# Performance work log

Measured on AMD Instinct MI355X. Metric: run time of the kernel, lower is better.

## Reference

```python
import jax, jax.numpy as jnp
import numpy as np

LOOKBACK = 512
T = 131072
FEES = 0.00025


def setup_inputs() -> dict:
    key = jax.random.key(0)
    k1, k2, k3, k4 = jax.random.split(key, 4)
    features = jax.random.normal(k1, (T,), dtype=jnp.float32)
    # gross per-step asset returns near 1.0 (hourly price relatives)
    asset_returns = 1.0 + 0.01 * jax.random.normal(k2, (T,), dtype=jnp.float32)
    theta = jax.random.uniform(k3, (LOOKBACK + 2,), dtype=jnp.float32)  # torch.rand init
    p_init = jax.random.uniform(k4, (LOOKBACK - 1,), dtype=jnp.float32)  # the lookback-1 seed positions
    return {"features": features, "asset_returns": asset_returns, "theta": theta, "p_init": p_init}


def _positions(features, theta, p_init):
    lb = theta.shape[0] - 2
    n_steps = features.shape[0] - lb + 1
    # all sliding windows features[t-lb:t], t = lb..T  -> [n_steps, lb]
    idx = jnp.arange(n_steps)[:, None] + jnp.arange(lb)[None, :]
    win = features[idx]
    wmean = win.mean(axis=1, keepdims=True)
    wstd = jnp.std(win, axis=1, ddof=1, keepdims=True)  # torch.std is unbiased
    win_norm = (win - wmean) / wstd

    # running stats over ALL positions so far (growing list in the original)
    n0 = jnp.asarray(p_init.shape[0], dtype=jnp.float32)
    state0 = (n0, p_init.sum(), jnp.sum(p_init * p_init), p_init[-1])

    one = jnp.ones((1,), dtype=features.dtype)

    def step(state, w):
        n, s, ss, p_last = state
        mean = s / n
        std = jnp.sqrt((ss - n * mean * mean) / (n - 1.0))
        last_norm = (p_last - mean) / std
        xt = jnp.concatenate([w, last_norm[None], one])  # [lb+2]
        xt = (xt - xt.mean()) / jnp.std(xt, ddof=1)
        p_new = jax.nn.sigmoid(jnp.dot(theta, xt))
        return (n + 1.0, s + p_new, ss + p_new * p_new, p_new), p_new

    _, p_seq = jax.lax.scan(step, state0, win_norm)
    return jnp.concatenate([p_init, p_seq])  # length T


def _bot_returns(P, asset_returns, fees):
    inv0 = P[0]
    cash0 = 1.0 - inv0

    def step(state, rp):
        inv, cash = state
        r, p = rp
        inv = inv * r
        pv = inv + cash
        delta = pv * p - inv  # desired - current investment
        inv = inv + jnp.where(delta > 0, delta * (1.0 - fees), delta)
        cash = cash + jnp.where(delta > 0, -delta, -delta * (1.0 - fees))
        return (inv, cash), inv + cash

    _, pv_tail = jax.lax.scan(step, (inv0, cash0), (asset_returns[1:], P[1:]))
    pv = jnp.concatenate([jnp.ones((1,), dtype=pv_tail.dtype), pv_tail])  # length T
    ratios = pv[1:] / pv[:-1]
    return jnp.concatenate([jnp.ones((1,), dtype=ratios.dtype), ratios])


def reference(features, asset_returns, theta, p_init):
    P = _positions(features, theta, p_init)
    return _bot_returns(P, asset_returns, FEES)
```

## Files before the change

kernel.cpp:

```cpp
#include <hip/hip_runtime.h>
#include <math.h>

#define T_TOTAL 131072
#define LB      512
#define NSTEPS  130561
#define NPAD    130564
#define OMF     0.99975f
#define KC     -1.4426950408889634f

#define OFF_E    0
#define OFF_P0   (NPAD)
#define OFF_P    (2*NPAD)
#define OFF_BS   (2*NPAD + T_TOTAL)
#define OFF_BSS  (OFF_BS + 2048)
#define OFF_CP   (OFF_BSS + 2048)

static __device__ __forceinline__ float fast_rcp(float x) {
#if __has_builtin(__builtin_amdgcn_rcpf)
    return __builtin_amdgcn_rcpf(x);
#else
    return 1.0f / x;
#endif
}
static __device__ __forceinline__ float fast_rsq(float x) {
#if __has_builtin(__builtin_amdgcn_rsqf)
    return __builtin_amdgcn_rsqf(x);
#else
    return 1.0f / sqrtf(x);
#endif
}
static __device__ __forceinline__ float fast_exp2(float x) {
#if __has_builtin(__builtin_amdgcn_exp2f)
    return __builtin_amdgcn_exp2f(x);
#else
    return exp2f(x);
#endif
}

__global__ __launch_bounds__(256, 1) void precompute_kernel(
    const float* __restrict__ features,
    const float* __restrict__ theta,
    const float* __restrict__ p_init,
    float* __restrict__ e_out,
    float* __restrict__ p0_out,
    float* __restrict__ P,
    float* __restrict__ bs,
    float* __restrict__ bss,
    float* __restrict__ cpool)
{
    __shared__ float f_lds[1536];
    __shared__ float th_lds[512];
    const int tid = threadIdx.x;
    const int b   = blockIdx.x;
    const int base = b * 1024;

    {
        const float4* fg = (const float4*)features;
        float4* f4s = (float4*)f_lds;
        int g0 = b * 256 + tid; g0 = g0 > 32767 ? 32767 : g0;
        f4s[tid] = fg[g0];
        if (tid < 128) {
            int g1 = b * 256 + 256 + tid; g1 = g1 > 32767 ? 32767 : g1;
            f4s[256 + tid] = fg[g1];
        }
        const float4* tg = (const float4*)theta;
        float4* t4s = (float4*)th_lds;
        if (tid >= 128 && tid < 256) t4s[tid - 128] = tg[tid - 128];
    }
    if (b == 0) {
        P[tid] = p_init[tid < 511 ? tid : 510];
        if (tid + 256 < 511) P[tid + 256] = p_init[tid + 256];
    }
    __syncthreads();

    float thsum = 0.f;
    {
        int l6 = tid & 63;
#pragma unroll
        for (int j = 0; j < 8; ++j) thsum += th_lds[l6 + 64 * j];
#pragma unroll
        for (int d = 32; d; d >>= 1) thsum += __shfl_xor(thsum, d, 64);
    }

    const float4* f4 = (const float4*)f_lds;
    const float4* t4 = (const float4*)th_lds;

    float d0 = 0.f, d1 = 0.f, d2 = 0.f, d3 = 0.f;
    float fsum0 = 0.f, fss0 = 0.f;
    float4 a = f4[tid];
    const float a00 = a.x, a01 = a.y, a02 = a.z;
#pragma unroll 4
    for (int j = 0; j < 128; ++j) {
        float4 bb = f4[tid + j + 1];
        float4 th = t4[j];
        d0 = fmaf(th.x, a.x, d0); d0 = fmaf(th.y, a.y, d0);
        d0 = fmaf(th.z, a.z, d0); d0 = fmaf(th.w, a.w, d0);
        d1 = fmaf(th.x, a.y, d1); d1 = fmaf(th.y, a.z, d1);
        d1 = fmaf(th.z, a.w, d1); d1 = fmaf(th.w, bb.x, d1);
        d2 = fmaf(th.x, a.z, d2); d2 = fmaf(th.y, a.w, d2);
        d2 = fmaf(th.z, bb.x, d2); d2 = fmaf(th.w, bb.y, d2);
        d3 = fmaf(th.x, a.w, d3); d3 = fmaf(th.y, bb.x, d3);
        d3 = fmaf(th.z, bb.y, d3); d3 = fmaf(th.w, bb.z, d3);
        fsum0 += (a.x + a.y) + (a.z + a.w);
        fss0 = fmaf(a.x, a.x, fss0); fss0 = fmaf(a.y, a.y, fss0);
        fss0 = fmaf(a.z, a.z, fss0); fss0 = fmaf(a.w, a.w, fss0);
        a = bb;
    }
    const float b00 = a.x, b01 = a.y, b02 = a.z;
    const float fsum1 = fsum0 - a00 + b00;
    const float fsum2 = fsum1 - a01 + b01;
    const float fsum3 = fsum2 - a02 + b02;
    float fss1 = fss0 - a00 * a00; fss1 = fmaf(b00, b00, fss1);
    float fss2 = fss1 - a01 * a01; fss2 = fmaf(b01, b01, fss2);
    float fss3 = fss2 - a02 * a02; fss3 = fmaf(b02, b02, fss3);

    const float th512 = theta[512];
    const float th513 = theta[513];
    const float sall  = thsum + th512 + th513;
    const float A_    = (512.0f - 1.0f / 514.0f) / 513.0f;
    const float rsqA  = fast_rsq(A_);
    const float cE    = th513 - sall * (1.0f / 514.0f);
    if (b == 0 && tid == 0) cpool[0] = KC * (th512 - sall * (1.0f / 514.0f));

    float ez[4], pv[4];
    const float fs_[4] = { fsum0, fsum1, fsum2, fsum3 };
    const float fq_[4] = { fss0,  fss1,  fss2,  fss3  };
    const float dd_[4] = { d0, d1, d2, d3 };
#pragma unroll
    for (int c = 0; c < 4; ++c) {
        float m    = fs_[c] * (1.0f / 512.0f);
        float varw = (fq_[c] - fs_[c] * m) * (1.0f / 511.0f);
        float dn   = (dd_[c] - m * thsum) * fast_rsq(varw);
        ez[c] = KC * (dn + cE);
        pv[c] = fast_rcp(1.0f + fast_exp2(ez[c] * rsqA));
    }

    const int t4i = base + 4 * tid;
    if (t4i + 3 < NSTEPS) {
        ((float4*)e_out)[b * 256 + tid]  = make_float4(ez[0], ez[1], ez[2], ez[3]);
        ((float4*)p0_out)[b * 256 + tid] = make_float4(pv[0], pv[1], pv[2], pv[3]);
    } else {
#pragma unroll
        for (int c = 0; c < 4; ++c)
            if (t4i + c < NSTEPS) { e_out[t4i + c] = ez[c]; p0_out[t4i + c] = pv[c]; }
    }

    float c1 = 0.f, c2 = 0.f;
#pragma unroll
    for (int c = 0; c < 4; ++c) {
        float p = (t4i + c < NSTEPS) ? pv[c] : 0.f;
        c1 += p; c2 = fmaf(p, p, c2);
    }
#pragma unroll
    for (int d = 8; d; d >>= 1) {
        c1 += __shfl_down(c1, d, 16);
        c2 += __shfl_down(c2, d, 16);
    }
    if ((tid & 15) == 0) {
        int idx = b * 16 + (tid >> 4);
        bs[idx] = c1; bss[idx] = c2;
    }
}

__global__ __launch_bounds__(64, 1) void pos_kernel(
    const float* __restrict__ p_init,
    const float* __restrict__ e,
    const float* __restrict__ p0,
    const float* __restrict__ bs,
    const float* __restrict__ bss,
    const float* __restrict__ cpool,
    float* __restrict__ P)
{
    const int l = threadIdx.x;
    const int b = blockIdx.x;
    const int g = b * 64 + l;

    float sa = 0.f, qa = 0.f;
    for (int j = l; j < 511; j += 64) { float v = p_init[j]; sa += v; qa = fmaf(v, v, qa); }
#pragma unroll
    for (int d = 32; d; d >>= 1) { sa += __shfl_xor(sa, d, 64); qa += __shfl_xor(qa, d, 64); }

    float ba = 0.f, ca = 0.f;
    for (int j = l; j < b * 64; j += 64) { ba += bs[j]; ca += bss[j]; }
#pragma unroll
    for (int d = 32; d; d >>= 1) { ba += __shfl_xor(ba, d, 64); ca += __shfl_xor(ca, d, 64); }

    float vb = bs[g], vc = bss[g];
    float ib = vb, ic = vc;
#pragma unroll
    for (int d = 1; d < 64; d <<= 1) {
        float ub = __shfl_up(ib, d, 64);
        float uc = __shfl_up(ic, d, 64);
        if (l >= d) { ib += ub; ic += uc; }
    }
    float s  = sa + ba + (ib - vb);
    float ss = qa + ca + (ic - vc);

    if (g > 2040) return;

    const float Gp = cpool[0];
    const float A_ = (512.0f - 1.0f / 514.0f) / 513.0f;
    const float B_ = (1.0f - 1.0f / 514.0f) / 513.0f;
    const float C_ = -2.0f / (514.0f * 513.0f);

    const int k0   = g * 64;
    const int kend = (k0 + 64 < NSTEPS) ? k0 + 64 : NSTEPS;
    const int kw   = (g == 0) ? 0 : k0 - 12;

    float plast = (g == 0) ? p_init[510] : p0[k0 - 13];
    float nf    = 511.0f + (float)k0;
    float rnm1  = fast_rcp(nf - 1.0f);
    const float mean_f = s * fast_rcp(nf);
    const float rv_f   = fast_rsq(fmaf(-s, mean_f, ss) * rnm1);

    const float4* e4 = (const float4*)(e + kw);
    const int maxi = (NPAD / 4 - 1) - (kw >> 2);

    float4 er[19];
#pragma unroll
    for (int i = 0; i < 19; ++i) er[i] = e4[i < maxi ? i : maxi];

#define BSTEP(EK, I) { \
    float rn   = fast_rcp(nf); \
    float mean = s * rn; \
    float varp = fmaf(-s, mean, ss) * rnm1; \
    float rv   = fast_rsq(varp); \
    float u    = (plast - mean) * rv; \
    float vx   = fmaf(u, fmaf(B_, u, C_), A_); \
    float r2   = fast_rsq(vx); \
    float z    = fmaf(u, Gp, (EK)) * r2; \
    float w    = fast_exp2(z); \
    float pnew = fast_rcp(1.0f + w); \
    s += pnew; ss = fmaf(pnew, pnew, ss); plast = pnew; \
    rnm1 = rn; nf += 1.0f; \
    int k = kw + (I); \
    if (k < kend) P[511 + k] = pnew; }
#define BWARM(EK) { \
    float u  = (plast - mean_f) * rv_f; \
    float vx = fmaf(u, fmaf(B_, u, C_), A_); \
    float r2 = fast_rsq(vx); \
    float z  = fmaf(u, Gp, (EK)) * r2; \
    plast = fast_rcp(1.0f + fast_exp2(z)); }
#define B4(Q, IB) { BSTEP(Q.x, IB+0); BSTEP(Q.y, IB+1); BSTEP(Q.z, IB+2); BSTEP(Q.w, IB+3); }
#define W4(Q) { BWARM(Q.x); BWARM(Q.y); BWARM(Q.z); BWARM(Q.w); }

    if (g == 0) { B4(er[0], 0); B4(er[1], 4); B4(er[2], 8); }
    else        { W4(er[0]);    W4(er[1]);    W4(er[2]);    }
    B4(er[3], 12);  B4(er[4], 16);  B4(er[5], 20);  B4(er[6], 24);
    B4(er[7], 28);  B4(er[8], 32);  B4(er[9], 36);  B4(er[10],40);
    B4(er[11],44);  B4(er[12],48);  B4(er[13],52);  B4(er[14],56);
    B4(er[15],60);  B4(er[16],64);  B4(er[17],68);  B4(er[18],72);
#undef BSTEP
#undef BWARM
#undef B4
#undef W4
}

__global__ __launch_bounds__(64, 1) void port_kernel(
    const float* __restrict__ ar,
    const float* __restrict__ Pp,
    float* __restrict__ out)
{
    const int g = blockIdx.x * 64 + threadIdx.x;
    const int t0   = g * 32;
    const int t0w  = (g == 0) ? 1 : t0;
    const int tend = (t0 + 32 < T_TOTAL) ? t0 + 32 : T_TOTAL;
    const int tw   = (g == 0) ? 0 : t0 - 8;

    float x = Pp[(g == 0) ? 0 : (tw - 1)];
    float inv = x, cash = 1.0f - x, pvprev = 1.0f;
    if (g == 0) out[0] = 1.0f;

    const float4* P4 = (const float4*)(Pp + tw);
    const float4* A4 = (const float4*)(ar + tw);

    float4 pr[10], arr[10];
#pragma unroll
    for (int i = 0; i < 10; ++i) { pr[i] = P4[i]; arr[i] = A4[i]; }

#define CST(RR, PPV, I) { \
    int t = tw + (I); \
    if (t >= 1) { \
        float invn  = inv * (RR); \
        float pv    = invn + cash; \
        float delta = fmaf(pv, (PPV), -invn); \
        float dfee  = delta * OMF; \
        bool  pos   = delta > 0.0f; \
        inv  = invn + (pos ? dfee : delta); \
        cash = cash - (pos ? delta : dfee); \
        float pvn = inv + cash; \
        if (t >= t0w && t < tend) out[t] = pvn * fast_rcp(pvprev); \
        pvprev = pvn; } }
#define C4(PQ, AQ, IB) { CST(AQ.x, PQ.x, IB+0); CST(AQ.y, PQ.y, IB+1); \
                         CST(AQ.z, PQ.z, IB+2); CST(AQ.w, PQ.w, IB+3); }

    C4(pr[0], arr[0], 0);   C4(pr[1], arr[1], 4);
    C4(pr[2], arr[2], 8);   C4(pr[3], arr[3], 12);
    C4(pr[4], arr[4], 16);  C4(pr[5], arr[5], 20);
    C4(pr[6], arr[6], 24);  C4(pr[7], arr[7], 28);
    C4(pr[8], arr[8], 32);  C4(pr[9], arr[9], 36);
#undef CST
#undef C4
}

extern "C" void kernel_launch(void* const* d_in, const int* in_sizes, int n_in,
                              void* d_out, int out_size, void* d_ws, size_t ws_size,
                              hipStream_t stream) {
    const float* features      = (const float*)d_in[0];
    const float* asset_returns = (const float*)d_in[1];
    const float* theta         = (const float*)d_in[2];
    const float* p_init        = (const float*)d_in[3];
    float* out = (float*)d_out;
    float* ws  = (float*)d_ws;

    float* e_arr = ws + OFF_E;
    float* p0    = ws + OFF_P0;
    float* P     = ws + OFF_P;
    float* bs    = ws + OFF_BS;
    float* bss   = ws + OFF_BSS;
    float* cpool = ws + OFF_CP;

    precompute_kernel<<<128, 256, 0, stream>>>(features, theta, p_init,
                                               e_arr, p0, P, bs, bss, cpool);
    pos_kernel<<<32, 64, 0, stream>>>(p_init, e_arr, p0, bs, bss, cpool, P);
    port_kernel<<<64, 64, 0, stream>>>(asset_returns, P, out);
}
```

Measured before the change: 96.46 us.

## Split window dot product across two half-blocks and vectorize prefix reductions

The precompute kernel now has each block cover 512 outputs instead of 1024. The two 128-thread halves each handle half of the 512-tap window and combine their partial results through LDS. The grid doubles to 256 blocks so more CUs take part and each thread's serial loop is half as long. In pos_kernel, the p_init and block-sum reductions now use float4 loads instead of strided scalar loops. The trade-off is an extra LDS round trip and barrier, and half the threads sit idle during the epilogue.

```diff
diff --git a/kernel.cpp b/kernel.cpp
--- a/kernel.cpp
+++ b/kernel.cpp
@@ -48,24 +48,26 @@
     float* __restrict__ bss,
     float* __restrict__ cpool)
 {
-    __shared__ float f_lds[1536];
+    __shared__ float f_lds[1088];
     __shared__ float th_lds[512];
+    __shared__ float part_lds[128][7];
     const int tid = threadIdx.x;
     const int b   = blockIdx.x;
-    const int base = b * 1024;
+    const int q   = tid & 127;
+    const int h   = tid >> 7;
 
     {
         const float4* fg = (const float4*)features;
         float4* f4s = (float4*)f_lds;
-        int g0 = b * 256 + tid; g0 = g0 > 32767 ? 32767 : g0;
+        int g0 = b * 128 + tid; g0 = g0 > 32767 ? 32767 : g0;
         f4s[tid] = fg[g0];
-        if (tid < 128) {
-            int g1 = b * 256 + 256 + tid; g1 = g1 > 32767 ? 32767 : g1;
+        if (tid < 16) {
+            int g1 = b * 128 + 256 + tid; g1 = g1 > 32767 ? 32767 : g1;
             f4s[256 + tid] = fg[g1];
         }
         const float4* tg = (const float4*)theta;
         float4* t4s = (float4*)th_lds;
-        if (tid >= 128 && tid < 256) t4s[tid - 128] = tg[tid - 128];
+        if (h == 1) t4s[q] = tg[q];
     }
     if (b == 0) {
         P[tid] = p_init[tid < 511 ? tid : 510];
@@ -87,12 +89,12 @@
 
     float d0 = 0.f, d1 = 0.f, d2 = 0.f, d3 = 0.f;
     float fsum0 = 0.f, fss0 = 0.f;
-    float4 a = f4[tid];
-    const float a00 = a.x, a01 = a.y, a02 = a.z;
+    const int jt0 = 64 * h;
+    float4 a = f4[q + jt0];
 #pragma unroll 4
-    for (int j = 0; j < 128; ++j) {
-        float4 bb = f4[tid + j + 1];
-        float4 th = t4[j];
+    for (int j = 0; j < 64; ++j) {
+        float4 bb = f4[q + jt0 + j + 1];
+        float4 th = t4[jt0 + j];
         d0 = fmaf(th.x, a.x, d0); d0 = fmaf(th.y, a.y, d0);
         d0 = fmaf(th.z, a.z, d0); d0 = fmaf(th.w, a.w, d0);
         d1 = fmaf(th.x, a.y, d1); d1 = fmaf(th.y, a.z, d1);
@@ -106,59 +108,73 @@
         fss0 = fmaf(a.z, a.z, fss0); fss0 = fmaf(a.w, a.w, fss0);
         a = bb;
     }
-    const float b00 = a.x, b01 = a.y, b02 = a.z;
-    const float fsum1 = fsum0 - a00 + b00;
-    const float fsum2 = fsum1 - a01 + b01;
-    const float fsum3 = fsum2 - a02 + b02;
-    float fss1 = fss0 - a00 * a00; fss1 = fmaf(b00, b00, fss1);
-    float fss2 = fss1 - a01 * a01; fss2 = fmaf(b01, b01, fss2);
-    float fss3 = fss2 - a02 * a02; fss3 = fmaf(b02, b02, fss3);
-
-    const float th512 = theta[512];
-    const float th513 = theta[513];
-    const float sall  = thsum + th512 + th513;
-    const float A_    = (512.0f - 1.0f / 514.0f) / 513.0f;
-    const float rsqA  = fast_rsq(A_);
-    const float cE    = th513 - sall * (1.0f / 514.0f);
-    if (b == 0 && tid == 0) cpool[0] = KC * (th512 - sall * (1.0f / 514.0f));
-
-    float ez[4], pv[4];
-    const float fs_[4] = { fsum0, fsum1, fsum2, fsum3 };
-    const float fq_[4] = { fss0,  fss1,  fss2,  fss3  };
-    const float dd_[4] = { d0, d1, d2, d3 };
-#pragma unroll
-    for (int c = 0; c < 4; ++c) {
-        float m    = fs_[c] * (1.0f / 512.0f);
-        float varw = (fq_[c] - fs_[c] * m) * (1.0f / 511.0f);
-        float dn   = (dd_[c] - m * thsum) * fast_rsq(varw);
-        ez[c] = KC * (dn + cE);
-        pv[c] = fast_rcp(1.0f + fast_exp2(ez[c] * rsqA));
-    }
-
-    const int t4i = base + 4 * tid;
-    if (t4i + 3 < NSTEPS) {
-        ((float4*)e_out)[b * 256 + tid]  = make_float4(ez[0], ez[1], ez[2], ez[3]);
-        ((float4*)p0_out)[b * 256 + tid] = make_float4(pv[0], pv[1], pv[2], pv[3]);
-    } else {
-#pragma unroll
-        for (int c = 0; c < 4; ++c)
-            if (t4i + c < NSTEPS) { e_out[t4i + c] = ez[c]; p0_out[t4i + c] = pv[c]; }
-    }
-
-    float c1 = 0.f, c2 = 0.f;
-#pragma unroll
-    for (int c = 0; c < 4; ++c) {
-        float p = (t4i + c < NSTEPS) ? pv[c] : 0.f;
-        c1 += p; c2 = fmaf(p, p, c2);
-    }
-#pragma unroll
-    for (int d = 8; d; d >>= 1) {
-        c1 += __shfl_down(c1, d, 16);
-        c2 += __shfl_down(c2, d, 16);
-    }
-    if ((tid & 15) == 0) {
-        int idx = b * 16 + (tid >> 4);
-        bs[idx] = c1; bss[idx] = c2;
+
+    if (h == 1) {
+        part_lds[q][0] = d0; part_lds[q][1] = d1;
+        part_lds[q][2] = d2; part_lds[q][3] = d3;
+        part_lds[q][4] = fsum0; part_lds[q][5] = fss0;
+    }
+    __syncthreads();
+    if (h == 0) {
+        d0 += part_lds[q][0]; d1 += part_lds[q][1];
+        d2 += part_lds[q][2]; d3 += part_lds[q][3];
+        fsum0 += part_lds[q][4]; fss0 += part_lds[q][5];
+
+        const float a00 = f_lds[4*q + 0], a01 = f_lds[4*q + 1], a02 = f_lds[4*q + 2];
+        const float b00 = f_lds[4*q + 512], b01 = f_lds[4*q + 513], b02 = f_lds[4*q + 514];
+        const float fsum1 = fsum0 - a00 + b00;
+        const float fsum2 = fsum1 - a01 + b01;
+        const float fsum3 = fsum2 - a02 + b02;
+        float fss1 = fss0 - a00 * a00; fss1 = fmaf(b00, b00, fss1);
+        float fss2 = fss1 - a01 * a01; fss2 = fmaf(b01, b01, fss2);
+        float fss3 = fss2 - a02 * a02; fss3 = fmaf(b02, b02, fss3);
+
+        const float th512 = theta[512];
+        const float th513 = theta[513];
+        const float sall  = thsum + th512 + th513;
+        const float A_    = (512.0f - 1.0f / 514.0f) / 513.0f;
+        const float rsqA  = fast_rsq(A_);
+        const float cE    = th513 - sall * (1.0f / 514.0f);
+        if (b == 0 && tid == 0) cpool[0] = KC * (th512 - sall * (1.0f / 514.0f));
+
+        float ez[4], pv[4];
+        const float fs_[4] = { fsum0, fsum1, fsum2, fsum3 };
+        const float fq_[4] = { fss0,  fss1,  fss2,  fss3  };
+        const float dd_[4] = { d0, d1, d2, d3 };
+#pragma unroll
+        for (int c = 0; c < 4; ++c) {
+            float m    = fs_[c] * (1.0f / 512.0f);
+            float varw = (fq_[c] - fs_[c] * m) * (1.0f / 511.0f);
+            float dn   = (dd_[c] - m * thsum) * fast_rsq(varw);
+            ez[c] = KC * (dn + cE);
+            pv[c] = fast_rcp(1.0f + fast_exp2(ez[c] * rsqA));
+        }
+
+        const int t4i = b * 512 + 4 * q;
+        if (t4i + 3 < NSTEPS) {
+            ((float4*)e_out)[b * 128 + q]  = make_float4(ez[0], ez[1], ez[2], ez[3]);
+            ((float4*)p0_out)[b * 128 + q] = make_float4(pv[0], pv[1], pv[2], pv[3]);
+        } else {
+#pragma unroll
+            for (int c = 0; c < 4; ++c)
+                if (t4i + c < NSTEPS) { e_out[t4i + c] = ez[c]; p0_out[t4i + c] = pv[c]; }
+        }
+
+        float c1 = 0.f, c2 = 0.f;
+#pragma unroll
+        for (int c = 0; c < 4; ++c) {
+            float p = (t4i + c < NSTEPS) ? pv[c] : 0.f;
+            c1 += p; c2 = fmaf(p, p, c2);
+        }
+#pragma unroll
+        for (int d = 8; d; d >>= 1) {
+            c1 += __shfl_down(c1, d, 16);
+            c2 += __shfl_down(c2, d, 16);
+        }
+        if ((q & 15) == 0) {
+            int idx = b * 8 + (q >> 4);
+            bs[idx] = c1; bss[idx] = c2;
+        }
     }
 }
 
@@ -175,15 +191,37 @@
     const int b = blockIdx.x;
     const int g = b * 64 + l;
 
-    float sa = 0.f, qa = 0.f;
-    for (int j = l; j < 511; j += 64) { float v = p_init[j]; sa += v; qa = fmaf(v, v, qa); }
-#pragma unroll
-    for (int d = 32; d; d >>= 1) { sa += __shfl_xor(sa, d, 64); qa += __shfl_xor(qa, d, 64); }
+    float sa, qa;
+    {
+        const float4* p4 = (const float4*)p_init;
+        float4 v0 = p4[l];
+        float4 v1 = (l <= 62) ? p4[64 + l] : make_float4(0.f,0.f,0.f,0.f);
+        float  t0 = (l < 3) ? p_init[508 + l] : 0.f;
+        sa = ((v0.x + v0.y) + (v0.z + v0.w)) + ((v1.x + v1.y) + (v1.z + v1.w)) + t0;
+        qa = fmaf(v0.x, v0.x, v0.y * v0.y) + fmaf(v0.z, v0.z, v0.w * v0.w)
+           + fmaf(v1.x, v1.x, v1.y * v1.y) + fmaf(v1.z, v1.z, v1.w * v1.w)
+           + t0 * t0;
+#pragma unroll
+        for (int d = 32; d; d >>= 1) { sa += __shfl_xor(sa, d, 64); qa += __shfl_xor(qa, d, 64); }
+    }
 
     float ba = 0.f, ca = 0.f;
-    for (int j = l; j < b * 64; j += 64) { ba += bs[j]; ca += bss[j]; }
-#pragma unroll
-    for (int d = 32; d; d >>= 1) { ba += __shfl_xor(ba, d, 64); ca += __shfl_xor(ca, d, 64); }
+    {
+        const float4* b4 = (const float4*)bs;
+        const float4* c4 = (const float4*)bss;
+        const int lim = b * 16;
+#pragma unroll
+        for (int k = 0; k < 8; ++k) {
+            int idx = l + 64 * k;
+            bool v = idx < lim;
+            float4 vb4 = v ? b4[idx] : make_float4(0.f,0.f,0.f,0.f);
+            float4 vc4 = v ? c4[idx] : make_float4(0.f,0.f,0.f,0.f);
+            ba += (vb4.x + vb4.y) + (vb4.z + vb4.w);
+            ca += (vc4.x + vc4.y) + (vc4.z + vc4.w);
+        }
+#pragma unroll
+        for (int d = 32; d; d >>= 1) { ba += __shfl_xor(ba, d, 64); ca += __shfl_xor(ca, d, 64); }
+    }
 
     float vb = bs[g], vc = bss[g];
     float ib = vb, ic = vc;
@@ -320,7 +358,7 @@
     float* bss   = ws + OFF_BSS;
     float* cpool = ws + OFF_CP;
 
-    precompute_kernel<<<128, 256, 0, stream>>>(features, theta, p_init,
+    precompute_kernel<<<256, 256, 0, stream>>>(features, theta, p_init,
                                                e_arr, p0, P, bs, bss, cpool);
     pos_kernel<<<32, 64, 0, stream>>>(p_init, e_arr, p0, bs, bss, cpool, P);
     port_kernel<<<64, 64, 0, stream>>>(asset_returns, P, out);
```

New measurement: 84.77 us. 12.1% less time.
